# Kernel tuning notes

Hardware: AMD Instinct MI355X
Metric: run time of the kernel (lower is better)

Reference implementation:

```python
import jax, jax.numpy as jnp
import numpy as np

B, T, C, NH = 4, 2048, 1024, 16
HS = C // NH  # 64


def setup_inputs() -> dict:
    key = jax.random.key(0)
    ks = jax.random.split(key, 3)
    x = jax.random.normal(ks[0], (B, T, C), dtype=jnp.float32)
    w_attn = jax.random.normal(ks[1], (C, 3 * C), dtype=jnp.float32) * (1.0 / np.sqrt(C))
    b_attn = jnp.zeros((3 * C,), dtype=jnp.float32)
    w_proj = jax.random.normal(ks[2], (C, C), dtype=jnp.float32) * (1.0 / np.sqrt(C))
    b_proj = jnp.zeros((C,), dtype=jnp.float32)
    return {"x": x, "w_attn": w_attn, "b_attn": b_attn, "w_proj": w_proj, "b_proj": b_proj}


def reference(x, w_attn, b_attn, w_proj, b_proj):
    Bx, Tx, Cx = x.shape
    qkv = x @ w_attn + b_attn                      # (B,T,3C)
    q, k, v = jnp.split(qkv, 3, axis=2)
    # faithful to torch: view(B,T,hs,nh).transpose(1,3) -> (B,nh,hs,T)
    def to_heads(t):
        return jnp.transpose(t.reshape(Bx, Tx, HS, NH), (0, 3, 2, 1))
    q, k, v = to_heads(q), to_heads(k), to_heads(v)
    # att[b,h,i,j] = q_i . k_j / sqrt(hs)
    att = jnp.einsum('bhdi,bhdj->bhij', q, k) * (1.0 / np.sqrt(HS))
    # buffer is tril.T == upper-triangular; keep i<=j, mask i>j
    keep = jnp.triu(jnp.ones((Tx, Tx), dtype=bool))[None, None]
    att = jnp.where(keep, att, -jnp.inf)
    att = jax.nn.softmax(att, axis=-2)             # normalize over i
    y = jnp.einsum('bhdi,bhij->bhdj', v, att)      # (B,nh,hs,T)
    y = jnp.transpose(y, (0, 3, 2, 1)).reshape(Bx, Tx, Cx)
    return y @ w_proj + b_proj
```

## Files before the change

kernel.cpp:

```cpp
#include <hip/hip_runtime.h>
#include <stdint.h>


typedef __attribute__((ext_vector_type(8))) _Float16 f16x8;
typedef __attribute__((ext_vector_type(4))) _Float16 f16x4;
typedef __attribute__((ext_vector_type(2))) __fp16   fp16x2_t;
typedef __attribute__((ext_vector_type(4))) float    f32x4;

#define NT_   8192
#define NC_   1024
#define N3C_  3072

__device__ __forceinline__ uint32_t pkrtz(float a, float b){
  union { fp16x2_t h; uint32_t u; } cv;
  cv.h = __builtin_amdgcn_cvt_pkrtz(a, b);
  return cv.u;
}

__global__ void k_cvt(const float* __restrict__ src, _Float16* __restrict__ dst, int n4){
  int idx = blockIdx.x*blockDim.x + threadIdx.x;
  int stride = gridDim.x*blockDim.x;
  for (int i = idx; i < n4; i += stride){
    float4 v = ((const float4*)src)[i];
    f16x4 o;
    o[0] = (_Float16)v.x; o[1] = (_Float16)v.y;
    o[2] = (_Float16)v.z; o[3] = (_Float16)v.w;
    ((f16x4*)dst)[i] = o;
  }
}

__global__ void k_wattn_t(const float* __restrict__ w, _Float16* __restrict__ wt){
  int t = threadIdx.x;
  int m0 = blockIdx.x*128, c0 = blockIdx.y*32;
  int mcol = m0 + t;
  int part = mcol >> 10, rr = mcol & 1023;
  int mp = part*1024 + (rr & 15)*64 + (rr >> 4);
  alignas(16) _Float16 buf[32];
  #pragma unroll
  for (int cc = 0; cc < 32; cc++)
    buf[cc] = (_Float16)w[(size_t)(c0+cc)*N3C_ + mcol];
  uint4* dst = (uint4*)(wt + (size_t)mp*NC_ + c0);
  const uint4* sb = (const uint4*)buf;
  dst[0]=sb[0]; dst[1]=sb[1]; dst[2]=sb[2]; dst[3]=sb[3];
}

__global__ void k_wproj_t(const float* __restrict__ w, _Float16* __restrict__ wt){
  int t = threadIdx.x;
  int o0 = blockIdx.x*128, cp0 = blockIdx.y*32;
  int o = o0 + t;
  alignas(16) _Float16 buf[32];
  #pragma unroll
  for (int i = 0; i < 32; i++){
    int cp = cp0 + i;
    int row = (cp & 63)*16 + (cp >> 6);
    buf[i] = (_Float16)w[(size_t)row*NC_ + o];
  }
  uint4* dst = (uint4*)(wt + (size_t)o*NC_ + cp0);
  const uint4* sb = (const uint4*)buf;
  dst[0]=sb[0]; dst[1]=sb[1]; dst[2]=sb[2]; dst[3]=sb[3];
}

__global__ void k_bias(const float* __restrict__ ba, float* __restrict__ bp){
  int i = blockIdx.x*blockDim.x + threadIdx.x;
  int part = i >> 10, rr = i & 1023, h = rr >> 6, d = rr & 63;
  bp[i] = ba[part*1024 + d*16 + h];
}

template<int OUT_HALF>
__global__ __launch_bounds__(256) void k_gemm(
    const _Float16* __restrict__ A, const _Float16* __restrict__ BT,
    const float* __restrict__ bias, void* __restrict__ outp,
    int M, int N, int K)
{
  __shared__ _Float16 As[128][40];
  __shared__ _Float16 Bs[128][40];
  int tid = threadIdx.x;
  int wave = tid >> 6, lane = tid & 63;
  int wr = wave >> 1, wc = wave & 1;
  int g = lane >> 4, l15 = lane & 15;
  f32x4 acc[4][4] = {};
  const _Float16* Ag = A  + (size_t)blockIdx.y*128*K;
  const _Float16* Bg = BT + (size_t)blockIdx.x*128*K;
  int srow = tid >> 1, skoff = (tid & 1)*16;
  const _Float16* apt = Ag + (size_t)srow*K + skoff;
  const _Float16* bpt = Bg + (size_t)srow*K + skoff;
  uint4 ra0 = *(const uint4*)apt;
  uint4 ra1 = *(const uint4*)(apt + 8);
  uint4 rb0 = *(const uint4*)bpt;
  uint4 rb1 = *(const uint4*)(bpt + 8);
  for (int kt = 0; kt < K; kt += 32){
    __syncthreads();
    *(uint4*)&As[srow][skoff]     = ra0;
    *(uint4*)&As[srow][skoff + 8] = ra1;
    *(uint4*)&Bs[srow][skoff]     = rb0;
    *(uint4*)&Bs[srow][skoff + 8] = rb1;
    __syncthreads();
    if (kt + 32 < K){
      ra0 = *(const uint4*)(apt + kt + 32);
      ra1 = *(const uint4*)(apt + kt + 40);
      rb0 = *(const uint4*)(bpt + kt + 32);
      rb1 = *(const uint4*)(bpt + kt + 40);
    }
    f16x8 af[4], bf[4];
    #pragma unroll
    for (int mi = 0; mi < 4; mi++) af[mi] = *(const f16x8*)&As[wr*64 + mi*16 + l15][g*8];
    #pragma unroll
    for (int ni = 0; ni < 4; ni++) bf[ni] = *(const f16x8*)&Bs[wc*64 + ni*16 + l15][g*8];
    #pragma unroll
    for (int mi = 0; mi < 4; mi++)
      #pragma unroll
      for (int ni = 0; ni < 4; ni++)
        acc[mi][ni] = __builtin_amdgcn_mfma_f32_16x16x32_f16(af[mi], bf[ni], acc[mi][ni], 0, 0, 0);
  }
  int rowBase = blockIdx.y*128 + wr*64;
  int colBase = blockIdx.x*128 + wc*64;
  #pragma unroll
  for (int mi = 0; mi < 4; mi++){
    #pragma unroll
    for (int ni = 0; ni < 4; ni++){
      int col = colBase + ni*16 + l15;
      float bv = bias[col];
      #pragma unroll
      for (int r = 0; r < 4; r++){
        int row = rowBase + mi*16 + g*4 + r;
        float v = acc[mi][ni][r] + bv;
        if (OUT_HALF) ((_Float16*)outp)[(size_t)row*N + col] = (_Float16)v;
        else          ((float*)outp)[(size_t)row*N + col] = v;
      }
    }
  }
}

__global__ __launch_bounds__(256) void k_vt(const _Float16* __restrict__ qkv,
                                            _Float16* __restrict__ VT){
  __shared__ _Float16 ls[64][72];
  int bh = blockIdx.y, b = bh >> 4, h = bh & 15;
  int t0 = blockIdx.x*64;
  int tid = threadIdx.x;
  int trow = tid >> 2, doff = (tid & 3)*16;
  const _Float16* src = qkv + (size_t)(b*2048 + t0 + trow)*N3C_ + 2048 + h*64 + doff;
  *(uint4*)&ls[trow][doff]     = *(const uint4*)&src[0];
  *(uint4*)&ls[trow][doff + 8] = *(const uint4*)&src[8];
  __syncthreads();
  int drow = tid >> 2, toff = (tid & 3)*16;
  alignas(16) _Float16 buf[16];
  #pragma unroll
  for (int e = 0; e < 16; e++) buf[e] = ls[toff + e][drow];
  uint4* dst = (uint4*)(VT + ((size_t)bh*64 + drow)*2048 + t0 + toff);
  const uint4* sb = (const uint4*)buf;
  dst[0]=sb[0]; dst[1]=sb[1];
}

__global__ __launch_bounds__(256) void k_attn(
    const _Float16* __restrict__ qkv, const _Float16* __restrict__ VTb,
    _Float16* __restrict__ Y)
{
  __shared__ _Float16 Ks[64][72];
  __shared__ _Float16 Vs[64][72];
  __shared__ uint32_t Ps[4][16][32];
  int jtA = blockIdx.x;
  int jtB = 31 - jtA;
  int bh = blockIdx.y, b = bh >> 4, h = bh & 15;
  int tid = threadIdx.x, wave = tid >> 6, lane = tid & 63;
  int g = lane >> 4, l15 = lane & 15;
  uint32_t* Pw = &Ps[wave][0][0] + l15*32;
  int xm = (l15 & 7) << 2;

  int q0A = jtA*64 + wave*16, q0B = jtB*64 + wave*16;
  const _Float16* qA = qkv + (size_t)(b*2048 + q0A + l15)*N3C_ + 1024 + h*64;
  const _Float16* qB = qkv + (size_t)(b*2048 + q0B + l15)*N3C_ + 1024 + h*64;
  f16x8 qA0 = *(const f16x8*)&qA[g*8], qA1 = *(const f16x8*)&qA[32 + g*8];
  f16x8 qB0 = *(const f16x8*)&qB[g*8], qB1 = *(const f16x8*)&qB[32 + g*8];
  float mA = -3e30f, lA = 0.f, mB = -3e30f, lB = 0.f;
  f32x4 accA[4] = {}; f32x4 accB[4] = {};

  int srow = tid >> 2, soff = (tid & 3)*16;
  const _Float16* kbase = qkv + (size_t)(b*2048 + srow)*N3C_ + h*64 + soff;
  const _Float16* vbase = VTb + ((size_t)bh*64 + srow)*2048 + soff;

  auto process = [&](const f16x8& qf0, const f16x8& qf1, float& mrun, float& lrun,
                     f32x4* acc, int q0, int i0, bool diag){
    f32x4 s2[4];
    #pragma unroll
    for (int nb = 0; nb < 4; nb++){
      f16x8 kf0 = *(const f16x8*)&Ks[nb*16 + l15][g*8];
      f16x8 kf1 = *(const f16x8*)&Ks[nb*16 + l15][32 + g*8];
      f32x4 z = {};
      z = __builtin_amdgcn_mfma_f32_16x16x32_f16(kf0, qf0, z, 0, 0, 0);
      z = __builtin_amdgcn_mfma_f32_16x16x32_f16(kf1, qf1, z, 0, 0, 0);
      s2[nb] = z;
    }
    float p[4][4];
    #pragma unroll
    for (int nb = 0; nb < 4; nb++)
      #pragma unroll
      for (int r = 0; r < 4; r++)
        p[nb][r] = s2[nb][r]*0.125f;
    if (diag){
      int qidx = q0 + l15;
      #pragma unroll
      for (int nb = 0; nb < 4; nb++)
        #pragma unroll
        for (int r = 0; r < 4; r++){
          int kidx = i0 + nb*16 + g*4 + r;
          if (kidx > qidx) p[nb][r] = -3e30f;
        }
    }
    float mx = p[0][0];
    #pragma unroll
    for (int nb = 0; nb < 4; nb++)
      #pragma unroll
      for (int r = 0; r < 4; r++) mx = fmaxf(mx, p[nb][r]);
    mx = fmaxf(mx, __shfl_xor(mx, 16));
    mx = fmaxf(mx, __shfl_xor(mx, 32));
    float mnew = mrun;
    if (!__all(mx - mrun <= 8.0f)){
      mnew = fmaxf(mrun, mx);
      float alpha = __expf(mrun - mnew);
      lrun *= alpha;
      #pragma unroll
      for (int db = 0; db < 4; db++) acc[db] *= alpha;
    }
    float rs = 0.f;
    #pragma unroll
    for (int nb = 0; nb < 4; nb++)
      #pragma unroll
      for (int r = 0; r < 4; r++){
        float pv = __expf(p[nb][r] - mnew);
        p[nb][r] = pv;
        rs += pv;
      }
    rs += __shfl_xor(rs, 16);
    rs += __shfl_xor(rs, 32);
    lrun += rs;
    mrun = mnew;
    #pragma unroll
    for (int nb = 0; nb < 4; nb++)
      #pragma unroll
      for (int r2 = 0; r2 < 2; r2++){
        uint32_t u = pkrtz(p[nb][2*r2], p[nb][2*r2 + 1]);
        Pw[(nb*8 + g*2 + r2) ^ xm] = u;
      }
    #pragma unroll
    for (int ks = 0; ks < 2; ks++){
      f16x8 pb = *(const f16x8*)&Pw[(ks*16 + g*4) ^ xm];
      #pragma unroll
      for (int db = 0; db < 4; db++){
        f16x8 vb = *(const f16x8*)&Vs[db*16 + l15][ks*32 + g*8];
        acc[db] = __builtin_amdgcn_mfma_f32_16x16x32_f16(vb, pb, acc[db], 0, 0, 0);
      }
    }
  };

  uint4 ka0 = *(const uint4*)&kbase[0];
  uint4 ka1 = *(const uint4*)&kbase[8];
  uint4 va0 = *(const uint4*)&vbase[0];
  uint4 va1 = *(const uint4*)&vbase[8];
  for (int it = 0; it <= jtB; ++it){
    __syncthreads();
    *(uint4*)&Ks[srow][soff]     = ka0;
    *(uint4*)&Ks[srow][soff + 8] = ka1;
    *(uint4*)&Vs[srow][soff]     = va0;
    *(uint4*)&Vs[srow][soff + 8] = va1;
    if (it < jtB){
      size_t ko = (size_t)(it+1)*64*N3C_;
      int    vo = (it+1)*64;
      ka0 = *(const uint4*)&kbase[ko];
      ka1 = *(const uint4*)&kbase[ko + 8];
      va0 = *(const uint4*)&vbase[vo];
      va1 = *(const uint4*)&vbase[vo + 8];
    }
    __syncthreads();
    process(qB0, qB1, mB, lB, accB, q0B, it*64, it == jtB);
    if (it <= jtA) process(qA0, qA1, mA, lA, accA, q0A, it*64, it == jtA);
  }

  auto finish = [&](float lr, f32x4* acc, int q0){
    float inv = 1.0f / lr;
    _Float16* yb = Y + (size_t)(b*2048 + q0 + l15)*NC_ + h*64 + g*4;
    #pragma unroll
    for (int db = 0; db < 4; db++){
      f16x4 o;
      #pragma unroll
      for (int r = 0; r < 4; r++) o[r] = (_Float16)(acc[db][r]*inv);
      *(f16x4*)&yb[db*16] = o;
    }
  };
  finish(lA, accA, q0A);
  finish(lB, accB, q0B);
}

extern "C" void kernel_launch(void* const* d_in, const int* in_sizes, int n_in,
                              void* d_out, int out_size, void* d_ws, size_t ws_size,
                              hipStream_t stream)
{
  const float* x      = (const float*)d_in[0];
  const float* w_attn = (const float*)d_in[1];
  const float* b_attn = (const float*)d_in[2];
  const float* w_proj = (const float*)d_in[3];
  const float* b_proj = (const float*)d_in[4];
  float* out = (float*)d_out;
  char* ws = (char*)d_ws;
  _Float16* xb   = (_Float16*)(ws + 0);
  _Float16* wT   = (_Float16*)(ws + 16777216);
  _Float16* wpT  = (_Float16*)(ws + 23068672);
  float*    bp   = (float*)   (ws + 25165824);
  _Float16* qkv  = (_Float16*)(ws + 25178112);
  _Float16* VT   = (_Float16*)(ws + 75509760);
  _Float16* Y    = (_Float16*)(ws + 92286976);

  k_cvt<<<2048, 256, 0, stream>>>(x, xb, (NT_*NC_)/4);
  k_wattn_t<<<dim3(24, 32), 128, 0, stream>>>(w_attn, wT);
  k_wproj_t<<<dim3(8, 32), 128, 0, stream>>>(w_proj, wpT);
  k_bias<<<12, 256, 0, stream>>>(b_attn, bp);
  k_gemm<1><<<dim3(24, 64), 256, 0, stream>>>(xb, wT, bp, qkv, NT_, N3C_, NC_);
  k_vt<<<dim3(32, 64), 256, 0, stream>>>(qkv, VT);
  k_attn<<<dim3(16, 64), 256, 0, stream>>>(qkv, VT, Y);
  k_gemm<0><<<dim3(8, 64), 256, 0, stream>>>(Y, wpT, b_proj, out, NT_, NC_, NC_);
}
```

Before: 228.4 us.

## Fuse V transpose into QKV GEMM epilogue and use exp2 softmax with prescaled Q

The QKV GEMM epilogue now writes the V columns directly in transposed per-head layout, which removes the separate k_vt kernel and its extra pass over V. The attention kernel folds the 1/sqrt(d)*log2(e) scale into Q in fp16, uses exp2 instead of expf, raises the lazy-rescale threshold, sums row probabilities with packed fdot2 on the fp16 values, and uses a tree max reduction. The attention grid becomes 1D with heads interleaved, which changes block scheduling order. Scaling Q in fp16 and summing the rounded fp16 probabilities slightly alter numerics.

```diff
diff --git a/kernel.cpp b/kernel.cpp
--- a/kernel.cpp
+++ b/kernel.cpp
@@ -4,6 +4,7 @@
 
 typedef __attribute__((ext_vector_type(8))) _Float16 f16x8;
 typedef __attribute__((ext_vector_type(4))) _Float16 f16x4;
+typedef __attribute__((ext_vector_type(2))) _Float16 h2;
 typedef __attribute__((ext_vector_type(2))) __fp16   fp16x2_t;
 typedef __attribute__((ext_vector_type(4))) float    f32x4;
 
@@ -70,6 +71,7 @@
 __global__ __launch_bounds__(256) void k_gemm(
     const _Float16* __restrict__ A, const _Float16* __restrict__ BT,
     const float* __restrict__ bias, void* __restrict__ outp,
+    _Float16* __restrict__ VTout,
     int M, int N, int K)
 {
   __shared__ _Float16 As[128][40];
@@ -114,6 +116,26 @@
   }
   int rowBase = blockIdx.y*128 + wr*64;
   int colBase = blockIdx.x*128 + wc*64;
+  if (OUT_HALF && colBase >= 2048){
+    int b = rowBase >> 11;
+    int t0 = (rowBase & 2047);
+    #pragma unroll
+    for (int mi = 0; mi < 4; mi++){
+      #pragma unroll
+      for (int ni = 0; ni < 4; ni++){
+        int col = colBase + ni*16 + l15;
+        int cc = col - 2048;
+        int h = cc >> 6, d = cc & 63;
+        float bv = bias[col];
+        _Float16* dst = VTout + (((size_t)(b*16 + h)*64 + d)*2048) + t0 + mi*16 + g*4;
+        f16x4 o;
+        #pragma unroll
+        for (int r = 0; r < 4; r++) o[r] = (_Float16)(acc[mi][ni][r] + bv);
+        *(f16x4*)dst = o;
+      }
+    }
+    return;
+  }
   #pragma unroll
   for (int mi = 0; mi < 4; mi++){
     #pragma unroll
@@ -129,26 +151,6 @@
       }
     }
   }
-}
-
-__global__ __launch_bounds__(256) void k_vt(const _Float16* __restrict__ qkv,
-                                            _Float16* __restrict__ VT){
-  __shared__ _Float16 ls[64][72];
-  int bh = blockIdx.y, b = bh >> 4, h = bh & 15;
-  int t0 = blockIdx.x*64;
-  int tid = threadIdx.x;
-  int trow = tid >> 2, doff = (tid & 3)*16;
-  const _Float16* src = qkv + (size_t)(b*2048 + t0 + trow)*N3C_ + 2048 + h*64 + doff;
-  *(uint4*)&ls[trow][doff]     = *(const uint4*)&src[0];
-  *(uint4*)&ls[trow][doff + 8] = *(const uint4*)&src[8];
-  __syncthreads();
-  int drow = tid >> 2, toff = (tid & 3)*16;
-  alignas(16) _Float16 buf[16];
-  #pragma unroll
-  for (int e = 0; e < 16; e++) buf[e] = ls[toff + e][drow];
-  uint4* dst = (uint4*)(VT + ((size_t)bh*64 + drow)*2048 + t0 + toff);
-  const uint4* sb = (const uint4*)buf;
-  dst[0]=sb[0]; dst[1]=sb[1];
 }
 
 __global__ __launch_bounds__(256) void k_attn(
@@ -158,19 +160,22 @@
   __shared__ _Float16 Ks[64][72];
   __shared__ _Float16 Vs[64][72];
   __shared__ uint32_t Ps[4][16][32];
-  int jtA = blockIdx.x;
+  int bid = blockIdx.x;
+  int bh = bid & 63;
+  int jtA = bid >> 6;
   int jtB = 31 - jtA;
-  int bh = blockIdx.y, b = bh >> 4, h = bh & 15;
+  int b = bh >> 4, h = bh & 15;
   int tid = threadIdx.x, wave = tid >> 6, lane = tid & 63;
   int g = lane >> 4, l15 = lane & 15;
   uint32_t* Pw = &Ps[wave][0][0] + l15*32;
   int xm = (l15 & 7) << 2;
+  const _Float16 QS = (_Float16)0.18033688f;
 
   int q0A = jtA*64 + wave*16, q0B = jtB*64 + wave*16;
   const _Float16* qA = qkv + (size_t)(b*2048 + q0A + l15)*N3C_ + 1024 + h*64;
   const _Float16* qB = qkv + (size_t)(b*2048 + q0B + l15)*N3C_ + 1024 + h*64;
-  f16x8 qA0 = *(const f16x8*)&qA[g*8], qA1 = *(const f16x8*)&qA[32 + g*8];
-  f16x8 qB0 = *(const f16x8*)&qB[g*8], qB1 = *(const f16x8*)&qB[32 + g*8];
+  f16x8 qA0 = *(const f16x8*)&qA[g*8] * QS, qA1 = *(const f16x8*)&qA[32 + g*8] * QS;
+  f16x8 qB0 = *(const f16x8*)&qB[g*8] * QS, qB1 = *(const f16x8*)&qB[32 + g*8] * QS;
   float mA = -3e30f, lA = 0.f, mB = -3e30f, lB = 0.f;
   f32x4 accA[4] = {}; f32x4 accB[4] = {};
 
@@ -190,12 +195,12 @@
       z = __builtin_amdgcn_mfma_f32_16x16x32_f16(kf1, qf1, z, 0, 0, 0);
       s2[nb] = z;
     }
-    float p[4][4];
+    float p[16];
     #pragma unroll
     for (int nb = 0; nb < 4; nb++)
       #pragma unroll
       for (int r = 0; r < 4; r++)
-        p[nb][r] = s2[nb][r]*0.125f;
+        p[nb*4 + r] = s2[nb][r];
     if (diag){
       int qidx = q0 + l15;
       #pragma unroll
@@ -203,33 +208,41 @@
         #pragma unroll
         for (int r = 0; r < 4; r++){
           int kidx = i0 + nb*16 + g*4 + r;
-          if (kidx > qidx) p[nb][r] = -3e30f;
+          if (kidx > qidx) p[nb*4 + r] = -3e30f;
         }
     }
-    float mx = p[0][0];
-    #pragma unroll
-    for (int nb = 0; nb < 4; nb++)
-      #pragma unroll
-      for (int r = 0; r < 4; r++) mx = fmaxf(mx, p[nb][r]);
+    float t0 = fmaxf(fmaxf(p[0],  p[1]),  p[2]);
+    float t1 = fmaxf(fmaxf(p[3],  p[4]),  p[5]);
+    float t2 = fmaxf(fmaxf(p[6],  p[7]),  p[8]);
+    float t3 = fmaxf(fmaxf(p[9],  p[10]), p[11]);
+    float t4 = fmaxf(fmaxf(p[12], p[13]), p[14]);
+    float mx = fmaxf(fmaxf(fmaxf(t0, t1), t2), fmaxf(fmaxf(t3, t4), p[15]));
     mx = fmaxf(mx, __shfl_xor(mx, 16));
     mx = fmaxf(mx, __shfl_xor(mx, 32));
     float mnew = mrun;
-    if (!__all(mx - mrun <= 8.0f)){
+    if (!__all(mx - mrun <= 11.5f)){
       mnew = fmaxf(mrun, mx);
-      float alpha = __expf(mrun - mnew);
+      float alpha = __builtin_amdgcn_exp2f(mrun - mnew);
       lrun *= alpha;
       #pragma unroll
       for (int db = 0; db < 4; db++) acc[db] *= alpha;
     }
-    float rs = 0.f;
-    #pragma unroll
-    for (int nb = 0; nb < 4; nb++)
-      #pragma unroll
-      for (int r = 0; r < 4; r++){
-        float pv = __expf(p[nb][r] - mnew);
-        p[nb][r] = pv;
-        rs += pv;
-      }
+    uint32_t pk[8];
+    #pragma unroll
+    for (int i = 0; i < 8; i++){
+      float e0 = __builtin_amdgcn_exp2f(p[2*i]     - mnew);
+      float e1 = __builtin_amdgcn_exp2f(p[2*i + 1] - mnew);
+      pk[i] = pkrtz(e0, e1);
+    }
+    const h2 ones = { (_Float16)1.0f, (_Float16)1.0f };
+    union { uint32_t u; h2 h; } cv;
+    float rs0 = 0.f, rs1 = 0.f;
+    #pragma unroll
+    for (int i = 0; i < 4; i++){
+      cv.u = pk[i];     rs0 = __builtin_amdgcn_fdot2(cv.h, ones, rs0, false);
+      cv.u = pk[i + 4]; rs1 = __builtin_amdgcn_fdot2(cv.h, ones, rs1, false);
+    }
+    float rs = rs0 + rs1;
     rs += __shfl_xor(rs, 16);
     rs += __shfl_xor(rs, 32);
     lrun += rs;
@@ -237,10 +250,8 @@
     #pragma unroll
     for (int nb = 0; nb < 4; nb++)
       #pragma unroll
-      for (int r2 = 0; r2 < 2; r2++){
-        uint32_t u = pkrtz(p[nb][2*r2], p[nb][2*r2 + 1]);
-        Pw[(nb*8 + g*2 + r2) ^ xm] = u;
-      }
+      for (int r2 = 0; r2 < 2; r2++)
+        Pw[(nb*8 + g*2 + r2) ^ xm] = pk[nb*2 + r2];
     #pragma unroll
     for (int ks = 0; ks < 2; ks++){
       f16x8 pb = *(const f16x8*)&Pw[(ks*16 + g*4) ^ xm];
@@ -313,8 +324,7 @@
   k_wattn_t<<<dim3(24, 32), 128, 0, stream>>>(w_attn, wT);
   k_wproj_t<<<dim3(8, 32), 128, 0, stream>>>(w_proj, wpT);
   k_bias<<<12, 256, 0, stream>>>(b_attn, bp);
-  k_gemm<1><<<dim3(24, 64), 256, 0, stream>>>(xb, wT, bp, qkv, NT_, N3C_, NC_);
-  k_vt<<<dim3(32, 64), 256, 0, stream>>>(qkv, VT);
-  k_attn<<<dim3(16, 64), 256, 0, stream>>>(qkv, VT, Y);
-  k_gemm<0><<<dim3(8, 64), 256, 0, stream>>>(Y, wpT, b_proj, out, NT_, NC_, NC_);
-}
+  k_gemm<1><<<dim3(24, 64), 256, 0, stream>>>(xb, wT, bp, qkv, VT, NT_, N3C_, NC_);
+  k_attn<<<1024, 256, 0, stream>>>(qkv, VT, Y);
+  k_gemm<0><<<dim3(8, 64), 256, 0, stream>>>(Y, wpT, b_proj, out, (_Float16*)nullptr, NT_, NC_, NC_);
+}
```

Result: faster. 212.2 us (-7.1%).
